# Optimization experiments

Hardware: AMD Instinct MI355X
Metric: run time of the kernel (lower is better)

The kernel has to match this reference:

```python
import jax, jax.numpy as jnp
import numpy as np

H = 256; HID = 128; V = 50000; LV = 200
N = 512; L = 64; M = 64; C = 4; T = 8; K = 8; E = 2048


def _gru_cell(x, h, wih, whh, bih, bhh):
    gi = x @ wih.T + bih
    gh = h @ whh.T + bhh
    ir, iz, inn = jnp.split(gi, 3, -1)
    hr, hz, hn = jnp.split(gh, 3, -1)
    r = jax.nn.sigmoid(ir + hr)
    z = jax.nn.sigmoid(iz + hz)
    n = jnp.tanh(inn + r * hn)
    return (1.0 - z) * n + z * h


def _bigru(x, wih, whh, bih, bhh):
    # x: [B, L, D]; params stacked [2, ...] = (fwd, bwd). out [B, L, 2*hid]
    B = x.shape[0]
    hid = whh.shape[-1]
    def run(xseq, d):
        def step(h, xt):
            hn = _gru_cell(xt, h, wih[d], whh[d], bih[d], bhh[d])
            return hn, hn
        _, out = jax.lax.scan(step, jnp.zeros((B, hid), x.dtype), jnp.swapaxes(xseq, 0, 1))
        return jnp.swapaxes(out, 0, 1)
    fwd = run(x, 0)
    bwd = jnp.flip(run(jnp.flip(x, 1), 1), 1)
    return jnp.concatenate([fwd, bwd], -1)


def _attn_pool(x, w, b):
    # x: [..., L, H]; softmax over L (matches torch softmax(dim=0) per sequence)
    a = jnp.einsum('...lh,h->...l', x, w) + b
    wts = jax.nn.softmax(a, axis=-1)
    return jnp.einsum('...l,...lh->...h', wts, x)


def _forward(seq_emb, seq_wih, seq_whh, seq_bih, seq_bhh, seq_pw, seq_pb,
             ctx_wih, ctx_whh, ctx_bih, ctx_bhh, ctx_pw, ctx_pb,
             ast_label_tab, ast_tok_tab, ast_pw, ast_pb,
             tl_wiou, tl_biou, tl_uiou, tl_wf, tl_bf, tl_uf,
             fa_wih, fa_whh, fa_bih, fa_bhh, fa_aw, fa_ab,
             comb_w, comb_b, g1_w, g1_b, g2_w, g2_b,
             cls_w1, cls_b1, cls_w2, cls_b2,
             seq_tokens, ast_children, ast_child_mask, ast_label_ids, ast_tok_ids, ctx_nei, edges):
    n_stmt = seq_tokens.shape[1]
    # --- three sequence encoders (stmt/varname/vartype), vmapped over encoder axis
    def enc(toks, emb, wih, whh, bih, bhh, pw, pb):
        e = emb[toks]                              # [N, L, H]
        o = _bigru(e, wih, whh, bih, bhh)          # [N, L, H]
        return _attn_pool(o, pw, pb)               # [N, H]
    vecs = jax.vmap(enc)(seq_tokens, seq_emb, seq_wih, seq_whh, seq_bih, seq_bhh, seq_pw, seq_pb)
    stmt_v, varn_v, vart_v = vecs[0], vecs[1], vecs[2]
    # --- ChildSum TreeLSTM over AST, batched over statements, scanned by node index
    # (children always have lower index than parent -> valid topological order)
    tok_e = ast_tok_tab[ast_tok_ids].mean(2)       # [N, M, H]
    xn = 0.5 * ast_label_tab[ast_label_ids] + 0.5 * tok_e
    Mn = xn.shape[1]
    xs = jnp.swapaxes(xn, 0, 1)                    # [M, N, H]
    chs = jnp.swapaxes(ast_children, 0, 1)         # [M, N, C]
    cms = jnp.swapaxes(ast_child_mask, 0, 1).astype(xn.dtype)
    nidx = jnp.arange(xn.shape[0])[:, None]
    def tl_step(carry, inp):
        h_arr, c_arr = carry                       # [M, N, H] each
        m, x, ch, msk = inp
        ch_h = h_arr[ch, nidx] * msk[..., None]    # [N, C, H], masked children
        ch_c = c_arr[ch, nidx] * msk[..., None]
        h_sum = ch_h.sum(1)
        iou = x @ tl_wiou.T + tl_biou + h_sum @ tl_uiou.T
        i, o, u = jnp.split(iou, 3, -1)
        i = jax.nn.sigmoid(i); o = jax.nn.sigmoid(o); u = jnp.tanh(u)
        fg = jax.nn.sigmoid((x @ tl_wf.T + tl_bf)[:, None, :] + ch_h @ tl_uf.T)
        c = i * u + (fg * ch_c).sum(1)
        h = o * jnp.tanh(c)
        return (h_arr.at[m].set(h), c_arr.at[m].set(c)), None
    z0 = jnp.zeros((Mn, xn.shape[0], xn.shape[2]), xn.dtype)
    (h_arr, _), _ = jax.lax.scan(tl_step, (z0, z0), (jnp.arange(Mn), xs, chs, cms))
    ast_v = _attn_pool(jnp.swapaxes(h_arr, 0, 1), ast_pw, ast_pb)   # [N, H]
    # --- context encoder over neighbor statement vectors (detached in original)
    ctx_in = jax.lax.stop_gradient(stmt_v)[ctx_nei]                 # [N, K, H]
    ctx_v = _attn_pool(_bigru(ctx_in, ctx_wih, ctx_whh, ctx_bih, ctx_bhh), ctx_pw, ctx_pb)
    # --- feature attention over the 5 per-statement feature vectors
    feats = jnp.stack([stmt_v, ast_v, varn_v, vart_v, ctx_v], axis=1)  # [N, 5, H]
    o = _bigru(feats, fa_wih, fa_whh, fa_bih, fa_bhh)
    wts = jax.nn.softmax(o @ fa_aw + fa_ab, axis=-1)
    x = jnp.einsum('nl,nlh->nh', wts, feats)
    # --- neighbor-mean combine (undirected unique edges)
    e0, e1 = edges[:, 0], edges[:, 1]
    rows = jnp.concatenate([e0, e1]); srcs = jnp.concatenate([e1, e0])
    nei_sum = jax.ops.segment_sum(x[srcs], rows, num_segments=n_stmt)
    deg = jax.ops.segment_sum(jnp.ones(rows.shape[0], x.dtype), rows, num_segments=n_stmt)
    nei_mean = nei_sum / jnp.maximum(deg, 1.0)[:, None]
    x2 = jax.nn.relu(jnp.concatenate([x, nei_mean], -1) @ comb_w.T + comb_b)
    # --- 2-layer symmetric-normalized GCN (edges both directions + self loops)
    sl = jnp.arange(n_stmt)
    r2 = jnp.concatenate([e0, e1, sl]); c2 = jnp.concatenate([e1, e0, sl])
    d2 = jax.ops.segment_sum(jnp.ones(r2.shape[0], x.dtype), r2, num_segments=n_stmt)
    dis = jnp.maximum(d2, 1.0) ** -0.5
    norm = (dis[r2] * dis[c2])[:, None]
    spmm = lambda y: jax.ops.segment_sum(norm * y[c2], r2, num_segments=n_stmt)
    h1 = jax.nn.relu(spmm(x2 @ g1_w.T + g1_b))
    h2 = jax.nn.relu(spmm(h1 @ g2_w.T + g2_b))
    gvec = jnp.concatenate([h2.mean(0), h2.max(0)], -1)
    return (jax.nn.relu(gvec @ cls_w1.T + cls_b1) @ cls_w2.T + cls_b2)[0]


def setup_inputs() -> dict:
    rng = np.random.default_rng(0)
    ks = iter(jax.random.split(jax.random.key(0), 64))
    def p(shape, s=0.05):
        return jax.random.normal(next(ks), shape, dtype=jnp.float32) * s
    inp = {}
    inp['seq_tokens'] = jnp.asarray(rng.integers(0, V, (3, N, L)), jnp.int32)
    ub = np.maximum(np.arange(M), 1)
    inp['ast_children'] = jnp.asarray((rng.random((N, M, C)) * ub[None, :, None]).astype(np.int64), jnp.int32)
    inp['ast_child_mask'] = jnp.asarray((rng.random((N, M, C)) < 0.7) & (np.arange(M)[None, :, None] > 0))
    inp['ast_label_ids'] = jnp.asarray(rng.integers(0, LV, (N, M)), jnp.int32)
    inp['ast_tok_ids'] = jnp.asarray(rng.integers(0, V, (N, M, T)), jnp.int32)
    inp['ctx_nei'] = jnp.asarray(rng.integers(0, N, (N, K)), jnp.int32)
    pairs = rng.integers(0, N, (8 * E, 2))
    pairs = pairs[pairs[:, 0] < pairs[:, 1]]
    pairs = np.unique(pairs, axis=0)[:E]
    inp['edges'] = jnp.asarray(pairs, jnp.int32)
    inp['seq_emb'] = p((3, V, H)).at[:, 0].set(0.0)  # padding_idx=0
    inp['seq_wih'] = p((3, 2, 3 * HID, H)); inp['seq_whh'] = p((3, 2, 3 * HID, HID))
    inp['seq_bih'] = p((3, 2, 3 * HID)); inp['seq_bhh'] = p((3, 2, 3 * HID))
    inp['seq_pw'] = p((3, H)); inp['seq_pb'] = p((3,))
    inp['ctx_wih'] = p((2, 3 * HID, H)); inp['ctx_whh'] = p((2, 3 * HID, HID))
    inp['ctx_bih'] = p((2, 3 * HID)); inp['ctx_bhh'] = p((2, 3 * HID))
    inp['ctx_pw'] = p((H,)); inp['ctx_pb'] = p(())
    inp['ast_label_tab'] = p((LV, H)); inp['ast_tok_tab'] = p((V, H))
    inp['ast_pw'] = p((H,)); inp['ast_pb'] = p(())
    inp['tl_wiou'] = p((3 * H, H)); inp['tl_biou'] = p((3 * H,)); inp['tl_uiou'] = p((3 * H, H))
    inp['tl_wf'] = p((H, H)); inp['tl_bf'] = p((H,)); inp['tl_uf'] = p((H, H))
    inp['fa_wih'] = p((2, 3 * HID, H)); inp['fa_whh'] = p((2, 3 * HID, HID))
    inp['fa_bih'] = p((2, 3 * HID)); inp['fa_bhh'] = p((2, 3 * HID))
    inp['fa_aw'] = p((H,)); inp['fa_ab'] = p(())
    inp['comb_w'] = p((H, 2 * H)); inp['comb_b'] = p((H,))
    inp['g1_w'] = p((H, H)); inp['g1_b'] = p((H,))
    inp['g2_w'] = p((H, H)); inp['g2_b'] = p((H,))
    inp['cls_w1'] = p((H, 2 * H)); inp['cls_b1'] = p((H,))
    inp['cls_w2'] = p((1, H)); inp['cls_b2'] = p((1,))
    return inp


def reference(seq_emb, seq_wih, seq_whh, seq_bih, seq_bhh, seq_pw, seq_pb,
              ctx_wih, ctx_whh, ctx_bih, ctx_bhh, ctx_pw, ctx_pb,
              ast_label_tab, ast_tok_tab, ast_pw, ast_pb,
              tl_wiou, tl_biou, tl_uiou, tl_wf, tl_bf, tl_uf,
              fa_wih, fa_whh, fa_bih, fa_bhh, fa_aw, fa_ab,
              comb_w, comb_b, g1_w, g1_b, g2_w, g2_b,
              cls_w1, cls_b1, cls_w2, cls_b2,
              seq_tokens, ast_children, ast_child_mask, ast_label_ids, ast_tok_ids, ctx_nei, edges):
    return _forward(seq_emb, seq_wih, seq_whh, seq_bih, seq_bhh, seq_pw, seq_pb,
                    ctx_wih, ctx_whh, ctx_bih, ctx_bhh, ctx_pw, ctx_pb,
                    ast_label_tab, ast_tok_tab, ast_pw, ast_pb,
                    tl_wiou, tl_biou, tl_uiou, tl_wf, tl_bf, tl_uf,
                    fa_wih, fa_whh, fa_bih, fa_bhh, fa_aw, fa_ab,
                    comb_w, comb_b, g1_w, g1_b, g2_w, g2_b,
                    cls_w1, cls_b1, cls_w2, cls_b2,
                    seq_tokens, ast_children, ast_child_mask, ast_label_ids, ast_tok_ids, ctx_nei, edges)
```

## Files before the change

### kernel.cpp

```cpp
#include <hip/hip_runtime.h>
#include <hip/hip_bf16.h>
#include <cmath>


__device__ __forceinline__ float sigf(float x) { return 1.f / (1.f + expf(-x)); }
__device__ __forceinline__ float b2f(__hip_bfloat16 x) { return __bfloat162float(x); }
__device__ __forceinline__ float bu2f(unsigned short u) {
  union { float f; unsigned i; } v; v.i = ((unsigned)u) << 16; return v.f;
}

typedef __attribute__((ext_vector_type(8))) short bf16x8v;
typedef __attribute__((ext_vector_type(4))) float f32x4;

__device__ __forceinline__ void gload16(const __hip_bfloat16* g, __hip_bfloat16* l) {
  __builtin_amdgcn_global_load_lds((const __attribute__((address_space(1))) void*)g,
                                   (__attribute__((address_space(3))) void*)l, 16, 0, 0);
}

__global__ __launch_bounds__(256) void k_build_wx(const float* __restrict__ wiou,
                                                  const float* __restrict__ wf,
                                                  const float* __restrict__ biou,
                                                  const float* __restrict__ bf,
                                                  float* __restrict__ w,
                                                  float* __restrict__ b) {
  int i = blockIdx.x * 256 + threadIdx.x;
  if (i < 1024 * 256) {
    int j = i >> 8, k = i & 255;
    w[i] = (j < 768) ? wiou[j * 256 + k] : wf[(j - 768) * 256 + k];
  }
  if (i < 1024) b[i] = (i < 768) ? biou[i] : bf[i - 768];
}

__global__ __launch_bounds__(256) void k_build_wproj(const float* __restrict__ uiou,
                                                     const float* __restrict__ uf,
                                                     float* __restrict__ w) {
  int i = blockIdx.x * 256 + threadIdx.x;
  if (i >= 1024 * 256) return;
  int j = i >> 8, k = i & 255;
  w[i] = (j < 768) ? uiou[j * 256 + k] : uf[(j - 768) * 256 + k];
}

__global__ __launch_bounds__(256) void k_zero_misc(float* __restrict__ nei_sum,
                                                   int* __restrict__ deg,
                                                   int* __restrict__ flag) {
  int i = blockIdx.x * 256 + threadIdx.x;
  if (i < 512 * 256) nei_sum[i] = 0.f;
  if (i < 512) deg[i] = 0;
  if (i == 0) *flag = 0;
}

__global__ __launch_bounds__(256) void k_mask_detect(const unsigned* __restrict__ raw,
                                                     int* __restrict__ flag) {
  int i = blockIdx.x * 256 + threadIdx.x;
  if (i < 32768) {
    if (raw[i] > 1u) atomicOr(flag, 1);
  }
}

__global__ __launch_bounds__(256) void k_mask_convert(const void* __restrict__ raw,
                                                      const int* __restrict__ flag,
                                                      int* __restrict__ msk) {
  int i = blockIdx.x * 256 + threadIdx.x;
  if (i >= 512 * 64 * 4) return;
  int v;
  if (*flag) v = ((const unsigned char*)raw)[i] != 0;
  else       v = ((const int*)raw)[i] != 0;
  msk[i] = v;
}

__global__ __launch_bounds__(256) void k_cvt_bf16(const float* __restrict__ A,
                                                  const int* __restrict__ ridx,
                                                  int rstride,
                                                  __hip_bfloat16* __restrict__ out) {
  int r = blockIdx.x * 8 + (threadIdx.x >> 5);
  int k = (threadIdx.x & 31) * 8;
  const float* src = A + (size_t)(ridx ? ridx[r] : r) * rstride + k;
  float4 v0 = *(const float4*)src;
  float4 v1 = *(const float4*)(src + 4);
  union { ushort4 u; __hip_bfloat16 b[4]; } p0, p1;
  p0.b[0] = __float2bfloat16(v0.x); p0.b[1] = __float2bfloat16(v0.y);
  p0.b[2] = __float2bfloat16(v0.z); p0.b[3] = __float2bfloat16(v0.w);
  p1.b[0] = __float2bfloat16(v1.x); p1.b[1] = __float2bfloat16(v1.y);
  p1.b[2] = __float2bfloat16(v1.z); p1.b[3] = __float2bfloat16(v1.w);
  __hip_bfloat16* dst = out + (size_t)r * 256 + k;
  *(ushort4*)dst = p0.u;
  *(ushort4*)(dst + 4) = p1.u;
}

__global__ __launch_bounds__(256) void k_gemm_mfma(const __hip_bfloat16* __restrict__ A,
                                                   const __hip_bfloat16* __restrict__ W,
                                                   const float* __restrict__ bias,
                                                   void* __restrict__ Cv,
                                                   int R, int K, int J,
                                                   int relu, int out_bf16) {
  __shared__ __align__(16) __hip_bfloat16 As[128 * 32];
  __shared__ __align__(16) __hip_bfloat16 Bs[128 * 32];
  int njt = J >> 7;
  int rt = blockIdx.x / njt;
  int jt = blockIdx.x - rt * njt;
  int tid = threadIdx.x;
  int w = tid >> 6, lane = tid & 63;
  int wr = w >> 1, wc = w & 1;

  const __hip_bfloat16* ga = A + (size_t)(rt * 128 + w * 32 + (lane >> 2)) * K + (lane & 3) * 8;
  const __hip_bfloat16* gb = W + (size_t)(jt * 128 + w * 32 + (lane >> 2)) * K + (lane & 3) * 8;
  __hip_bfloat16* lA0 = As + w * 1024;
  __hip_bfloat16* lB0 = Bs + w * 1024;
  size_t gstep16 = (size_t)16 * K;

  f32x4 acc[4][4];
#pragma unroll
  for (int m = 0; m < 4; ++m)
#pragma unroll
    for (int n = 0; n < 4; ++n) acc[m][n] = (f32x4){0.f, 0.f, 0.f, 0.f};

  int fr = lane & 15;
  int kg = (lane >> 4) * 8;
  const __hip_bfloat16* raA = As + (size_t)(wr * 64 + fr) * 32 + kg;
  const __hip_bfloat16* raB = Bs + (size_t)(wc * 64 + fr) * 32 + kg;

  for (int k0 = 0; k0 < K; k0 += 32) {
    __syncthreads();
    gload16(ga, lA0);
    gload16(ga + gstep16, lA0 + 512);
    gload16(gb, lB0);
    gload16(gb + gstep16, lB0 + 512);
    ga += 32; gb += 32;
    __syncthreads();
    bf16x8v a[4], b[4];
#pragma unroll
    for (int m = 0; m < 4; ++m) a[m] = *(const bf16x8v*)(raA + m * 512);
#pragma unroll
    for (int n = 0; n < 4; ++n) b[n] = *(const bf16x8v*)(raB + n * 512);
#pragma unroll
    for (int m = 0; m < 4; ++m)
#pragma unroll
      for (int n = 0; n < 4; ++n)
        acc[m][n] = __builtin_amdgcn_mfma_f32_16x16x32_bf16(a[m], b[n], acc[m][n], 0, 0, 0);
  }

  int row0 = rt * 128 + wr * 64 + (lane >> 4) * 4;
  int col0 = jt * 128 + wc * 64 + fr;
#pragma unroll
  for (int n = 0; n < 4; ++n) {
    int col = col0 + n * 16;
    float bv = bias ? bias[col] : 0.f;
#pragma unroll
    for (int m = 0; m < 4; ++m) {
#pragma unroll
      for (int j = 0; j < 4; ++j) {
        float v = acc[m][n][j] + bv;
        if (relu) v = fmaxf(v, 0.f);
        size_t idx = (size_t)(row0 + m * 16 + j) * J + col;
        if (out_bf16) ((__hip_bfloat16*)Cv)[idx] = __float2bfloat16(v);
        else ((float*)Cv)[idx] = v;
      }
    }
  }
}

__global__ __launch_bounds__(256) void k_gemm128(const float* __restrict__ A,
                                                 const int* __restrict__ ridx,
                                                 int rstride,
                                                 const float* __restrict__ W,
                                                 const float* __restrict__ bias,
                                                 float* __restrict__ C,
                                                 int R, int K, int J, int relu,
                                                 int out_bf16) {
  __shared__ float As[16][132];
  __shared__ float Ws[16][132];
  int njt = J >> 7;
  int rt = blockIdx.x / njt;
  int jt = blockIdx.x % njt;
  int tid = threadIdx.x;
  int tx = tid & 15, ty = tid >> 4;

  int row2 = tid >> 1;
  int kq = (tid & 1) * 4;
  int gr = rt * 128 + row2;
  const float* arow = A + (size_t)(ridx ? ridx[gr] : gr) * rstride;
  const float* wrow = W + (size_t)(jt * 128 + row2) * K;

  float acc[8][8];
#pragma unroll
  for (int i = 0; i < 8; ++i)
#pragma unroll
    for (int j = 0; j < 8; ++j) acc[i][j] = 0.f;

  for (int k0 = 0; k0 < K; k0 += 16) {
    float4 av0 = *(const float4*)(arow + k0 + kq);
    float4 av1 = *(const float4*)(arow + k0 + kq + 8);
    float4 wv0 = *(const float4*)(wrow + k0 + kq);
    float4 wv1 = *(const float4*)(wrow + k0 + kq + 8);
    __syncthreads();
    As[kq + 0][row2] = av0.x; As[kq + 1][row2] = av0.y;
    As[kq + 2][row2] = av0.z; As[kq + 3][row2] = av0.w;
    As[kq + 8][row2] = av1.x; As[kq + 9][row2] = av1.y;
    As[kq + 10][row2] = av1.z; As[kq + 11][row2] = av1.w;
    Ws[kq + 0][row2] = wv0.x; Ws[kq + 1][row2] = wv0.y;
    Ws[kq + 2][row2] = wv0.z; Ws[kq + 3][row2] = wv0.w;
    Ws[kq + 8][row2] = wv1.x; Ws[kq + 9][row2] = wv1.y;
    Ws[kq + 10][row2] = wv1.z; Ws[kq + 11][row2] = wv1.w;
    __syncthreads();
#pragma unroll
    for (int kk = 0; kk < 16; ++kk) {
      float a[8], b[8];
      *(float4*)&a[0] = *(const float4*)&As[kk][ty * 4];
      *(float4*)&a[4] = *(const float4*)&As[kk][64 + ty * 4];
      *(float4*)&b[0] = *(const float4*)&Ws[kk][tx * 4];
      *(float4*)&b[4] = *(const float4*)&Ws[kk][64 + tx * 4];
#pragma unroll
      for (int i = 0; i < 8; ++i)
#pragma unroll
        for (int j = 0; j < 8; ++j) acc[i][j] += a[i] * b[j];
    }
  }

  int col0 = jt * 128 + tx * 4;
  int col1 = jt * 128 + 64 + tx * 4;
  float b0[4], b1[4];
#pragma unroll
  for (int j = 0; j < 4; ++j) {
    b0[j] = bias ? bias[col0 + j] : 0.f;
    b1[j] = bias ? bias[col1 + j] : 0.f;
  }
#pragma unroll
  for (int i = 0; i < 8; ++i) {
    int row = rt * 128 + ((i < 4) ? (ty * 4 + i) : (64 + ty * 4 + i - 4));
    float v0[4], v1[4];
#pragma unroll
    for (int j = 0; j < 4; ++j) {
      float x0 = acc[i][j] + b0[j];
      float x1 = acc[i][j + 4] + b1[j];
      if (relu) { x0 = fmaxf(x0, 0.f); x1 = fmaxf(x1, 0.f); }
      v0[j] = x0; v1[j] = x1;
    }
    if (out_bf16) {
      __hip_bfloat16* Cb = (__hip_bfloat16*)C;
      union { ushort4 u; __hip_bfloat16 b[4]; } p0, p1;
#pragma unroll
      for (int j = 0; j < 4; ++j) { p0.b[j] = __float2bfloat16(v0[j]); p1.b[j] = __float2bfloat16(v1[j]); }
      *(ushort4*)(Cb + (size_t)row * J + col0) = p0.u;
      *(ushort4*)(Cb + (size_t)row * J + col1) = p1.u;
    } else {
      *(float4*)(C + (size_t)row * J + col0) = *(float4*)v0;
      *(float4*)(C + (size_t)row * J + col1) = *(float4*)v1;
    }
  }
}

__global__ __launch_bounds__(512) void k_gru4(const __hip_bfloat16* __restrict__ gi,
                                              const __hip_bfloat16* __restrict__ whhb,
                                              const float* __restrict__ bhh,
                                              float* __restrict__ out,
                                              int L) {
  __shared__ __align__(16) __hip_bfloat16 hsb[16][136];
  __shared__ float outl[16][392];
  int tid = threadIdx.x;
  int d = blockIdx.y;
  int n0 = blockIdx.x * 16;
  int w = tid >> 6, lane = tid & 63;
  int fr = lane & 15;
  int kg = (lane >> 4) * 8;
  int jw = w * 48;

  bf16x8v bfr[3][4];
  const __hip_bfloat16* wb = whhb + (size_t)d * 384 * 128;
#pragma unroll
  for (int cf = 0; cf < 3; ++cf)
#pragma unroll
    for (int kf = 0; kf < 4; ++kf)
      bfr[cf][kf] = *(const bf16x8v*)(wb + (size_t)(jw + cf * 16 + fr) * 128 + kf * 32 + kg);

  int s = tid >> 5;
  int j0 = (tid & 31) * 4;
  const float* bh = bhh + d * 384;
  float4 br = *(const float4*)(bh + j0);
  float4 bz = *(const float4*)(bh + 128 + j0);
  float4 bn = *(const float4*)(bh + 256 + j0);

  float h[4] = {0.f, 0.f, 0.f, 0.f};
  for (int i = tid; i < 16 * 136; i += 512) ((__hip_bfloat16*)hsb)[i] = __float2bfloat16(0.f);
  __syncthreads();

  int t = d ? (L - 1) : 0;
  int dt = d ? -1 : 1;

  for (int step = 0; step < L; ++step, t += dt) {
    const __hip_bfloat16* g = gi + (size_t)((n0 + s) * L + t) * 768 + d * 384 + j0;
    ushort4 gr4 = *(const ushort4*)(g);
    ushort4 gz4 = *(const ushort4*)(g + 128);
    ushort4 gn4 = *(const ushort4*)(g + 256);

    f32x4 acc[3];
#pragma unroll
    for (int cf = 0; cf < 3; ++cf) acc[cf] = (f32x4){0.f, 0.f, 0.f, 0.f};
#pragma unroll
    for (int kf = 0; kf < 4; ++kf) {
      bf16x8v a = *(const bf16x8v*)(&hsb[fr][kf * 32 + kg]);
#pragma unroll
      for (int cf = 0; cf < 3; ++cf)
        acc[cf] = __builtin_amdgcn_mfma_f32_16x16x32_bf16(a, bfr[cf][kf], acc[cf], 0, 0, 0);
    }
    int r0 = (lane >> 4) * 4;
#pragma unroll
    for (int cf = 0; cf < 3; ++cf) {
      int col = jw + cf * 16 + fr;
#pragma unroll
      for (int r = 0; r < 4; ++r) outl[r0 + r][col] = acc[cf][r];
    }
    __syncthreads();

    float4 sr = *(const float4*)&outl[s][j0];
    float4 sz = *(const float4*)&outl[s][128 + j0];
    float4 sn = *(const float4*)&outl[s][256 + j0];
    float gr[4] = {bu2f(gr4.x), bu2f(gr4.y), bu2f(gr4.z), bu2f(gr4.w)};
    float gz[4] = {bu2f(gz4.x), bu2f(gz4.y), bu2f(gz4.z), bu2f(gz4.w)};
    float gn[4] = {bu2f(gn4.x), bu2f(gn4.y), bu2f(gn4.z), bu2f(gn4.w)};
    float srv[4] = {sr.x, sr.y, sr.z, sr.w};
    float szv[4] = {sz.x, sz.y, sz.z, sz.w};
    float snv[4] = {sn.x, sn.y, sn.z, sn.w};
    float brv[4] = {br.x, br.y, br.z, br.w};
    float bzv[4] = {bz.x, bz.y, bz.z, bz.w};
    float bnv[4] = {bn.x, bn.y, bn.z, bn.w};
#pragma unroll
    for (int j = 0; j < 4; ++j) {
      float r = sigf(gr[j] + srv[j] + brv[j]);
      float z = sigf(gz[j] + szv[j] + bzv[j]);
      float nn = tanhf(gn[j] + r * (snv[j] + bnv[j]));
      h[j] = (1.f - z) * nn + z * h[j];
    }
    *(float4*)(out + (size_t)((n0 + s) * L + t) * 256 + d * 128 + j0) =
        (float4){h[0], h[1], h[2], h[3]};
    union { ushort4 u; __hip_bfloat16 b[4]; } hp;
#pragma unroll
    for (int j = 0; j < 4; ++j) hp.b[j] = __float2bfloat16(h[j]);
    *(ushort4*)&hsb[s][j0] = hp.u;
    __syncthreads();
  }
}

__global__ __launch_bounds__(256) void k_attn_pool(const float* __restrict__ score_src,
                                                   int s_ns, int s_ls,
                                                   const float* __restrict__ val_src,
                                                   int v_ns, int v_ls,
                                                   const float* __restrict__ w,
                                                   const float* __restrict__ bptr,
                                                   float* __restrict__ dst,
                                                   int dst_stride, int L) {
  __shared__ float wts[64];
  int n = blockIdx.x;
  int tid = threadIdx.x;
  if (tid < 64) {
    float a = -INFINITY;
    if (tid < L) {
      const float* row = score_src + (size_t)n * s_ns + (size_t)tid * s_ls;
      float s = bptr[0];
      for (int h = 0; h < 256; h += 4) {
        float4 v = *(const float4*)(row + h);
        float4 wv = *(const float4*)(w + h);
        s += v.x * wv.x + v.y * wv.y + v.z * wv.z + v.w * wv.w;
      }
      a = s;
    }
    float mx = a;
#pragma unroll
    for (int off = 32; off; off >>= 1) mx = fmaxf(mx, __shfl_xor(mx, off));
    float e = (tid < L) ? expf(a - mx) : 0.f;
    float ss = e;
#pragma unroll
    for (int off = 32; off; off >>= 1) ss += __shfl_xor(ss, off);
    if (tid < L) wts[tid] = e / ss;
  }
  __syncthreads();
  float acc = 0.f;
  for (int l = 0; l < L; ++l)
    acc += wts[l] * val_src[(size_t)n * v_ns + (size_t)l * v_ls + tid];
  dst[(size_t)n * dst_stride + tid] = acc;
}

__global__ __launch_bounds__(256) void k_xn_bf16(const float* __restrict__ label_tab,
                                                 const float* __restrict__ tok_tab,
                                                 const int* __restrict__ lbl_ids,
                                                 const int* __restrict__ tok_ids,
                                                 __hip_bfloat16* __restrict__ xnb) {
  int nm = blockIdx.x;
  int h = threadIdx.x;
  const int* tids = tok_ids + (size_t)nm * 8;
  float s = 0.f;
#pragma unroll
  for (int t = 0; t < 8; ++t) s += tok_tab[(size_t)tids[t] * 256 + h];
  float v = 0.5f * label_tab[(size_t)lbl_ids[nm] * 256 + h] + 0.0625f * s;
  xnb[(size_t)nm * 256 + h] = __float2bfloat16(v);
}

__global__ __launch_bounds__(256) void k_tl_combine4(const __hip_bfloat16* __restrict__ HU,
                                                     const __hip_bfloat16* __restrict__ XWALL,
                                                     const int* __restrict__ ch,
                                                     const int* __restrict__ msk,
                                                     float* __restrict__ h_arr,
                                                     float* __restrict__ c_arr,
                                                     __hip_bfloat16* __restrict__ hbf,
                                                     int m) {
  int n = blockIdx.x, h = threadIdx.x;
  const __hip_bfloat16* xw = XWALL + ((size_t)(n * 64 + m)) * 1024;
  float si = b2f(xw[h]), so = b2f(xw[256 + h]), su = b2f(xw[512 + h]);
  float xfv = b2f(xw[768 + h]);
  const int* chp = ch + ((size_t)(n * 64 + m)) * 4;
  const int* mkp = msk + ((size_t)(n * 64 + m)) * 4;
  float cs = 0.f;
#pragma unroll
  for (int c = 0; c < 4; ++c) {
    if (mkp[c]) {
      int cc = chp[c];
      const __hip_bfloat16* hu = HU + ((size_t)cc * 512 + n) * 1024;
      si += b2f(hu[h]);
      so += b2f(hu[256 + h]);
      su += b2f(hu[512 + h]);
      float fg = sigf(xfv + b2f(hu[768 + h]));
      cs += fg * c_arr[((size_t)cc * 512 + n) * 256 + h];
    }
  }
  float iv = sigf(si), ov = sigf(so), uv = tanhf(su);
  float cn = iv * uv + cs;
  float hn = ov * tanhf(cn);
  h_arr[((size_t)m * 512 + n) * 256 + h] = hn;
  c_arr[((size_t)m * 512 + n) * 256 + h] = cn;
  hbf[(size_t)n * 256 + h] = __float2bfloat16(hn);
}

__global__ __launch_bounds__(256) void k_edge_deg(const int* __restrict__ edges,
                                                  int* __restrict__ deg, int E) {
  int i = blockIdx.x * 256 + threadIdx.x;
  if (i < E) {
    atomicAdd(&deg[edges[2 * i]], 1);
    atomicAdd(&deg[edges[2 * i + 1]], 1);
  }
}

__global__ __launch_bounds__(256) void k_nei(const int* __restrict__ edges,
                                             const float* __restrict__ x,
                                             float* __restrict__ nei_sum) {
  int e = blockIdx.x, h = threadIdx.x;
  int a = edges[2 * e], b = edges[2 * e + 1];
  atomicAdd(&nei_sum[(size_t)a * 256 + h], x[(size_t)b * 256 + h]);
  atomicAdd(&nei_sum[(size_t)b * 256 + h], x[(size_t)a * 256 + h]);
}

__global__ __launch_bounds__(256) void k_xcat(const float* __restrict__ x,
                                              const float* __restrict__ nei_sum,
                                              const int* __restrict__ deg,
                                              float* __restrict__ xcat) {
  int n = blockIdx.x, h = threadIdx.x;
  xcat[(size_t)n * 512 + h] = x[(size_t)n * 256 + h];
  float d = fmaxf((float)deg[n], 1.f);
  xcat[(size_t)n * 512 + 256 + h] = nei_sum[(size_t)n * 256 + h] / d;
}

__global__ __launch_bounds__(256) void k_spmm_self(const float* __restrict__ y,
                                                   const int* __restrict__ deg,
                                                   float* __restrict__ ob) {
  int n = blockIdx.x, h = threadIdx.x;
  float dis2 = 1.f / (float)(deg[n] + 1);
  ob[(size_t)n * 256 + h] = dis2 * y[(size_t)n * 256 + h];
}

__global__ __launch_bounds__(256) void k_spmm_edge(const float* __restrict__ y,
                                                   const int* __restrict__ deg,
                                                   const int* __restrict__ edges,
                                                   float* __restrict__ ob) {
  int e = blockIdx.x, h = threadIdx.x;
  int a = edges[2 * e], b = edges[2 * e + 1];
  float w = (1.f / sqrtf((float)(deg[a] + 1))) * (1.f / sqrtf((float)(deg[b] + 1)));
  atomicAdd(&ob[(size_t)a * 256 + h], w * y[(size_t)b * 256 + h]);
  atomicAdd(&ob[(size_t)b * 256 + h], w * y[(size_t)a * 256 + h]);
}

__global__ __launch_bounds__(256) void k_relu_inplace(float* __restrict__ p) {
  int i = blockIdx.x * 256 + threadIdx.x;
  p[i] = fmaxf(p[i], 0.f);
}

__global__ __launch_bounds__(256) void k_final(const float* __restrict__ h2,
                                               const float* __restrict__ w1,
                                               const float* __restrict__ b1,
                                               const float* __restrict__ w2,
                                               const float* __restrict__ b2,
                                               float* __restrict__ outp) {
  __shared__ float gv[512];
  __shared__ float zz[256];
  int tid = threadIdx.x;
  float mn = 0.f, mx = -INFINITY;
  for (int n = 0; n < 512; ++n) {
    float v = h2[(size_t)n * 256 + tid];
    mn += v;
    mx = fmaxf(mx, v);
  }
  gv[tid] = mn / 512.f;
  gv[256 + tid] = mx;
  __syncthreads();
  float acc = b1[tid];
  for (int k = 0; k < 512; ++k) acc += gv[k] * w1[(size_t)tid * 512 + k];
  zz[tid] = fmaxf(acc, 0.f) * w2[tid];
  __syncthreads();
  for (int s = 128; s; s >>= 1) {
    if (tid < s) zz[tid] += zz[tid + s];
    __syncthreads();
  }
  if (tid == 0) outp[0] = zz[0] + b2[0];
}

extern "C" void kernel_launch(void* const* d_in, const int* in_sizes, int n_in,
                              void* d_out, int out_size, void* d_ws, size_t ws_size,
                              hipStream_t stream) {
  const int* seq_tokens    = (const int*)d_in[0];
  const int* ast_children  = (const int*)d_in[1];
  const void* ast_mask_raw = (const void*)d_in[2];
  const int* ast_label_ids = (const int*)d_in[3];
  const int* ast_tok_ids   = (const int*)d_in[4];
  const int* ctx_nei       = (const int*)d_in[5];
  const int* edges         = (const int*)d_in[6];
  const float* seq_emb  = (const float*)d_in[7];
  const float* seq_wih  = (const float*)d_in[8];
  const float* seq_whh  = (const float*)d_in[9];
  const float* seq_bih  = (const float*)d_in[10];
  const float* seq_bhh  = (const float*)d_in[11];
  const float* seq_pw   = (const float*)d_in[12];
  const float* seq_pb   = (const float*)d_in[13];
  const float* ctx_wih  = (const float*)d_in[14];
  const float* ctx_whh  = (const float*)d_in[15];
  const float* ctx_bih  = (const float*)d_in[16];
  const float* ctx_bhh  = (const float*)d_in[17];
  const float* ctx_pw   = (const float*)d_in[18];
  const float* ctx_pb   = (const float*)d_in[19];
  const float* ast_label_tab = (const float*)d_in[20];
  const float* ast_tok_tab   = (const float*)d_in[21];
  const float* ast_pw   = (const float*)d_in[22];
  const float* ast_pb   = (const float*)d_in[23];
  const float* tl_wiou  = (const float*)d_in[24];
  const float* tl_biou  = (const float*)d_in[25];
  const float* tl_uiou  = (const float*)d_in[26];
  const float* tl_wf    = (const float*)d_in[27];
  const float* tl_bf    = (const float*)d_in[28];
  const float* tl_uf    = (const float*)d_in[29];
  const float* fa_wih   = (const float*)d_in[30];
  const float* fa_whh   = (const float*)d_in[31];
  const float* fa_bih   = (const float*)d_in[32];
  const float* fa_bhh   = (const float*)d_in[33];
  const float* fa_aw    = (const float*)d_in[34];
  const float* fa_ab    = (const float*)d_in[35];
  const float* comb_w   = (const float*)d_in[36];
  const float* comb_b   = (const float*)d_in[37];
  const float* g1_w     = (const float*)d_in[38];
  const float* g1_b     = (const float*)d_in[39];
  const float* g2_w     = (const float*)d_in[40];
  const float* g2_b     = (const float*)d_in[41];
  const float* cls_w1   = (const float*)d_in[42];
  const float* cls_b1   = (const float*)d_in[43];
  const float* cls_w2   = (const float*)d_in[44];
  const float* cls_b2   = (const float*)d_in[45];
  float* outp = (float*)d_out;
  float* ws = (float*)d_ws;
  int E = in_sizes[6] / 2;

  size_t off = 0;
  auto take = [&](size_t n) { size_t o = off; off += n; return o; };
  const size_t F_FEATS = take(512 * 5 * 256);
  const size_t F_X     = take(512 * 256);
  const size_t F_X2    = take(512 * 256);
  const size_t F_Y     = take(512 * 256);
  const size_t F_H1    = take(512 * 256);
  const size_t F_H2    = take(512 * 256);
  const size_t F_XCAT  = take(512 * 512);
  const size_t F_NEI   = take(512 * 256);
  const size_t F_DEG   = take(512);
  const size_t F_FLAG  = take(16);
  const size_t F_MSK   = take(512 * 64 * 4);
  const size_t F_WXW   = take(1024 * 256);
  const size_t F_WXB   = take(1024);
  const size_t F_WPROJ = take(1024 * 256);
  const size_t F_REGION = take(83886080);
  (void)ws_size;

  float* FEATS = ws + F_FEATS;
  float* X     = ws + F_X;
  float* X2    = ws + F_X2;
  float* Y     = ws + F_Y;
  float* H1    = ws + F_H1;
  float* H2    = ws + F_H2;
  float* XCAT  = ws + F_XCAT;
  float* NEI   = ws + F_NEI;
  int*   DEG   = (int*)(ws + F_DEG);
  int*   FLAG  = (int*)(ws + F_FLAG);
  int*   MSK   = (int*)(ws + F_MSK);
  float* WXW   = ws + F_WXW;
  float* WXB   = ws + F_WXB;
  float* WPROJ = ws + F_WPROJ;
  float* REG   = ws + F_REGION;
  __hip_bfloat16* GI16  = (__hip_bfloat16*)REG;
  float* OUT   = REG + 13631488;
  __hip_bfloat16* XWALL16 = (__hip_bfloat16*)REG;
  float* HARR  = REG + 17000000;
  float* CARR  = REG + 25500000;
  __hip_bfloat16* HU16 = (__hip_bfloat16*)(REG + 34000000);
  __hip_bfloat16* GIFA16 = (__hip_bfloat16*)REG;
  float* OUTFA = REG + 1966080;
  __hip_bfloat16* ABF     = (__hip_bfloat16*)(REG + 60000000);
  __hip_bfloat16* WSEQBF  = (__hip_bfloat16*)(REG + 65000000);
  __hip_bfloat16* WCTXBF  = (__hip_bfloat16*)(REG + 65400000);
  __hip_bfloat16* WFABF   = (__hip_bfloat16*)(REG + 65600000);
  __hip_bfloat16* WXWBF   = (__hip_bfloat16*)(REG + 65800000);
  __hip_bfloat16* WPROJBF = (__hip_bfloat16*)(REG + 66100000);
  __hip_bfloat16* HBF     = (__hip_bfloat16*)(REG + 66500000);
  __hip_bfloat16* WHHSEQBF = (__hip_bfloat16*)(REG + 66600000);
  __hip_bfloat16* WHHCTXBF = (__hip_bfloat16*)(REG + 66800000);
  __hip_bfloat16* WHHFABF  = (__hip_bfloat16*)(REG + 66900000);

  auto gemm = [&](const float* A, const int* ridx, int rstride, const float* W,
                  const float* bias, float* C, int R, int K, int J, int relu,
                  int obf) {
    dim3 g((R / 128) * (J / 128));
    k_gemm128<<<g, 256, 0, stream>>>(A, ridx, rstride, W, bias, C, R, K, J, relu, obf);
  };
  auto cvt = [&](const float* A, const int* ridx, int rstride,
                 __hip_bfloat16* ob, int R) {
    k_cvt_bf16<<<R / 8, 256, 0, stream>>>(A, ridx, rstride, ob);
  };
  auto mgemm = [&](const __hip_bfloat16* A, const __hip_bfloat16* W,
                   const float* bias, void* C, int R, int K, int J, int relu,
                   int obf) {
    dim3 g((R / 128) * (J / 128));
    k_gemm_mfma<<<g, 256, 0, stream>>>(A, W, bias, C, R, K, J, relu, obf);
  };

  k_build_wx<<<1024, 256, 0, stream>>>(tl_wiou, tl_wf, tl_biou, tl_bf, WXW, WXB);
  k_build_wproj<<<1024, 256, 0, stream>>>(tl_uiou, tl_uf, WPROJ);
  k_zero_misc<<<512, 256, 0, stream>>>(NEI, DEG, FLAG);
  k_mask_detect<<<128, 256, 0, stream>>>((const unsigned*)ast_mask_raw, FLAG);
  k_mask_convert<<<512, 256, 0, stream>>>(ast_mask_raw, FLAG, MSK);
  cvt(seq_wih, nullptr, 256, WSEQBF, 2304);
  cvt(ctx_wih, nullptr, 256, WCTXBF, 768);
  cvt(fa_wih, nullptr, 256, WFABF, 768);
  cvt(WXW, nullptr, 256, WXWBF, 1024);
  cvt(WPROJ, nullptr, 256, WPROJBF, 1024);
  cvt(seq_whh, nullptr, 256, WHHSEQBF, 1152);
  cvt(ctx_whh, nullptr, 256, WHHCTXBF, 384);
  cvt(fa_whh, nullptr, 256, WHHFABF, 384);

  const int slot_of[3] = {0, 2, 3};
  for (int e = 0; e < 3; ++e) {
    cvt(seq_emb + (size_t)e * 50000 * 256, seq_tokens + (size_t)e * 32768, 256,
        ABF, 32768);
    mgemm(ABF, WSEQBF + (size_t)e * 768 * 256, seq_bih + (size_t)e * 768,
          GI16, 32768, 256, 768, 0, 1);
    k_gru4<<<dim3(32, 2), 512, 0, stream>>>(GI16, WHHSEQBF + (size_t)e * 2 * 384 * 128,
                                            seq_bhh + (size_t)e * 768, OUT, 64);
    k_attn_pool<<<512, 256, 0, stream>>>(OUT, 64 * 256, 256, OUT, 64 * 256, 256,
                                         seq_pw + e * 256, seq_pb + e,
                                         FEATS + slot_of[e] * 256, 1280, 64);
  }

  cvt(FEATS, ctx_nei, 1280, ABF, 4096);
  mgemm(ABF, WCTXBF, ctx_bih, GI16, 4096, 256, 768, 0, 1);
  k_gru4<<<dim3(32, 2), 512, 0, stream>>>(GI16, WHHCTXBF, ctx_bhh, OUT, 8);
  k_attn_pool<<<512, 256, 0, stream>>>(OUT, 8 * 256, 256, OUT, 8 * 256, 256,
                                       ctx_pw, ctx_pb, FEATS + 4 * 256, 1280, 8);

  k_xn_bf16<<<32768, 256, 0, stream>>>(ast_label_tab, ast_tok_tab, ast_label_ids,
                                       ast_tok_ids, ABF);
  mgemm(ABF, WXWBF, WXB, XWALL16, 32768, 256, 1024, 0, 1);
  for (int m = 0; m < 64; ++m) {
    k_tl_combine4<<<512, 256, 0, stream>>>(HU16, XWALL16, ast_children, MSK,
                                           HARR, CARR, HBF, m);
    if (m < 63)
      mgemm(HBF, WPROJBF, nullptr, HU16 + (size_t)m * 512 * 1024,
            512, 256, 1024, 0, 1);
  }
  k_attn_pool<<<512, 256, 0, stream>>>(HARR, 256, 512 * 256, HARR, 256, 512 * 256,
                                       ast_pw, ast_pb, FEATS + 1 * 256, 1280, 64);

  cvt(FEATS, nullptr, 256, ABF, 2560);
  mgemm(ABF, WFABF, fa_bih, GIFA16, 2560, 256, 768, 0, 1);
  k_gru4<<<dim3(32, 2), 512, 0, stream>>>(GIFA16, WHHFABF, fa_bhh, OUTFA, 5);
  k_attn_pool<<<512, 256, 0, stream>>>(OUTFA, 5 * 256, 256, FEATS, 1280, 256,
                                       fa_aw, fa_ab, X, 256, 5);

  k_edge_deg<<<(E + 255) / 256, 256, 0, stream>>>(edges, DEG, E);
  k_nei<<<E, 256, 0, stream>>>(edges, X, NEI);
  k_xcat<<<512, 256, 0, stream>>>(X, NEI, DEG, XCAT);
  gemm(XCAT, nullptr, 512, comb_w, comb_b, X2, 512, 512, 256, 1, 0);
  gemm(X2, nullptr, 256, g1_w, g1_b, Y, 512, 256, 256, 0, 0);
  k_spmm_self<<<512, 256, 0, stream>>>(Y, DEG, H1);
  k_spmm_edge<<<E, 256, 0, stream>>>(Y, DEG, edges, H1);
  k_relu_inplace<<<512, 256, 0, stream>>>(H1);
  gemm(H1, nullptr, 256, g2_w, g2_b, Y, 512, 256, 256, 0, 0);
  k_spmm_self<<<512, 256, 0, stream>>>(Y, DEG, H2);
  k_spmm_edge<<<E, 256, 0, stream>>>(Y, DEG, edges, H2);
  k_relu_inplace<<<512, 256, 0, stream>>>(H2);
  k_final<<<1, 256, 0, stream>>>(H2, cls_w1, cls_b1, cls_w2, cls_b2, outp);
}
```

Before: 2.101 ms.

## Batch three sequence-encoder GRUs into one launch with prefetch and fast activations

Input projections for all three sequence encoders are now computed into separate buffers, and one GRU kernel launch runs all three recurrences (96x2 blocks instead of three serial 32x2 launches). This fills more of the GPU's compute units during the latency-bound recurrent loop. The GRU loop also prefetches the next timestep's gate inputs, uses a lighter LDS-only barrier, and pads the shared output array. Sigmoid and tanh switch to fast-exp/rcp approximations in both the GRU and TreeLSTM kernels, trading a little accuracy for cheaper transcendentals, and the workspace grows to hold three projection and output buffers at once.

```diff
diff --git a/kernel.cpp b/kernel.cpp
--- a/kernel.cpp
+++ b/kernel.cpp
@@ -8,6 +8,14 @@
 __device__ __forceinline__ float bu2f(unsigned short u) {
   union { float f; unsigned i; } v; v.i = ((unsigned)u) << 16; return v.f;
 }
+__device__ __forceinline__ float fsig(float x) {
+  return __builtin_amdgcn_rcpf(1.f + __expf(-x));
+}
+__device__ __forceinline__ float ftanh(float x) {
+  float cx = fminf(fmaxf(x, -15.f), 15.f);
+  float e = __expf(2.f * cx);
+  return 1.f - 2.f * __builtin_amdgcn_rcpf(e + 1.f);
+}
 
 typedef __attribute__((ext_vector_type(8))) short bf16x8v;
 typedef __attribute__((ext_vector_type(4))) float f32x4;
@@ -15,6 +23,12 @@
 __device__ __forceinline__ void gload16(const __hip_bfloat16* g, __hip_bfloat16* l) {
   __builtin_amdgcn_global_load_lds((const __attribute__((address_space(1))) void*)g,
                                    (__attribute__((address_space(3))) void*)l, 16, 0, 0);
+}
+
+__device__ __forceinline__ void lds_barrier() {
+  asm volatile("s_waitcnt lgkmcnt(0)" ::: "memory");
+  __builtin_amdgcn_sched_barrier(0);
+  __builtin_amdgcn_s_barrier();
 }
 
 __global__ __launch_bounds__(256) void k_build_wx(const float* __restrict__ wiou,
@@ -249,16 +263,24 @@
   }
 }
 
-__global__ __launch_bounds__(512) void k_gru4(const __hip_bfloat16* __restrict__ gi,
+__global__ __launch_bounds__(512) void k_gru5(const __hip_bfloat16* __restrict__ gi,
                                               const __hip_bfloat16* __restrict__ whhb,
                                               const float* __restrict__ bhh,
                                               float* __restrict__ out,
-                                              int L) {
+                                              int L, int bpe,
+                                              unsigned gi_se, unsigned whh_se,
+                                              unsigned bhh_se, unsigned out_se) {
   __shared__ __align__(16) __hip_bfloat16 hsb[16][136];
-  __shared__ float outl[16][392];
+  __shared__ float outl[16][396];
   int tid = threadIdx.x;
   int d = blockIdx.y;
-  int n0 = blockIdx.x * 16;
+  int e = blockIdx.x / bpe;
+  int n0 = (blockIdx.x - e * bpe) * 16;
+  gi += (size_t)e * gi_se;
+  whhb += (size_t)e * whh_se;
+  bhh += (size_t)e * bhh_se;
+  out += (size_t)e * out_se;
+
   int w = tid >> 6, lane = tid & 63;
   int fr = lane & 15;
   int kg = (lane >> 4) * 8;
@@ -285,12 +307,20 @@
 
   int t = d ? (L - 1) : 0;
   int dt = d ? -1 : 1;
-
-  for (int step = 0; step < L; ++step, t += dt) {
-    const __hip_bfloat16* g = gi + (size_t)((n0 + s) * L + t) * 768 + d * 384 + j0;
-    ushort4 gr4 = *(const ushort4*)(g);
-    ushort4 gz4 = *(const ushort4*)(g + 128);
-    ushort4 gn4 = *(const ushort4*)(g + 256);
+  const __hip_bfloat16* gbase = gi + (size_t)(n0 + s) * L * 768 + d * 384 + j0;
+
+  const __hip_bfloat16* g0 = gbase + (size_t)t * 768;
+  ushort4 cr = *(const ushort4*)g0;
+  ushort4 cz = *(const ushort4*)(g0 + 128);
+  ushort4 cn4 = *(const ushort4*)(g0 + 256);
+
+  for (int step = 0; step < L; ++step) {
+    int tn = t + dt;
+    tn = (tn < 0) ? 0 : ((tn >= L) ? (L - 1) : tn);
+    const __hip_bfloat16* gn_ = gbase + (size_t)tn * 768;
+    ushort4 nr = *(const ushort4*)gn_;
+    ushort4 nz = *(const ushort4*)(gn_ + 128);
+    ushort4 nn4 = *(const ushort4*)(gn_ + 256);
 
     f32x4 acc[3];
 #pragma unroll
@@ -309,14 +339,14 @@
 #pragma unroll
       for (int r = 0; r < 4; ++r) outl[r0 + r][col] = acc[cf][r];
     }
-    __syncthreads();
+    lds_barrier();
 
     float4 sr = *(const float4*)&outl[s][j0];
     float4 sz = *(const float4*)&outl[s][128 + j0];
     float4 sn = *(const float4*)&outl[s][256 + j0];
-    float gr[4] = {bu2f(gr4.x), bu2f(gr4.y), bu2f(gr4.z), bu2f(gr4.w)};
-    float gz[4] = {bu2f(gz4.x), bu2f(gz4.y), bu2f(gz4.z), bu2f(gz4.w)};
-    float gn[4] = {bu2f(gn4.x), bu2f(gn4.y), bu2f(gn4.z), bu2f(gn4.w)};
+    float grv[4] = {bu2f(cr.x), bu2f(cr.y), bu2f(cr.z), bu2f(cr.w)};
+    float gzv[4] = {bu2f(cz.x), bu2f(cz.y), bu2f(cz.z), bu2f(cz.w)};
+    float gnv[4] = {bu2f(cn4.x), bu2f(cn4.y), bu2f(cn4.z), bu2f(cn4.w)};
     float srv[4] = {sr.x, sr.y, sr.z, sr.w};
     float szv[4] = {sz.x, sz.y, sz.z, sz.w};
     float snv[4] = {sn.x, sn.y, sn.z, sn.w};
@@ -325,9 +355,9 @@
     float bnv[4] = {bn.x, bn.y, bn.z, bn.w};
 #pragma unroll
     for (int j = 0; j < 4; ++j) {
-      float r = sigf(gr[j] + srv[j] + brv[j]);
-      float z = sigf(gz[j] + szv[j] + bzv[j]);
-      float nn = tanhf(gn[j] + r * (snv[j] + bnv[j]));
+      float r = fsig(grv[j] + srv[j] + brv[j]);
+      float z = fsig(gzv[j] + szv[j] + bzv[j]);
+      float nn = ftanh(gnv[j] + r * (snv[j] + bnv[j]));
       h[j] = (1.f - z) * nn + z * h[j];
     }
     *(float4*)(out + (size_t)((n0 + s) * L + t) * 256 + d * 128 + j0) =
@@ -336,7 +366,10 @@
 #pragma unroll
     for (int j = 0; j < 4; ++j) hp.b[j] = __float2bfloat16(h[j]);
     *(ushort4*)&hsb[s][j0] = hp.u;
-    __syncthreads();
+    lds_barrier();
+
+    cr = nr; cz = nz; cn4 = nn4;
+    t += dt;
   }
 }
 
@@ -417,13 +450,13 @@
       si += b2f(hu[h]);
       so += b2f(hu[256 + h]);
       su += b2f(hu[512 + h]);
-      float fg = sigf(xfv + b2f(hu[768 + h]));
+      float fg = fsig(xfv + b2f(hu[768 + h]));
       cs += fg * c_arr[((size_t)cc * 512 + n) * 256 + h];
     }
   }
-  float iv = sigf(si), ov = sigf(so), uv = tanhf(su);
+  float iv = fsig(si), ov = fsig(so), uv = ftanh(su);
   float cn = iv * uv + cs;
-  float hn = ov * tanhf(cn);
+  float hn = ov * ftanh(cn);
   h_arr[((size_t)m * 512 + n) * 256 + h] = hn;
   c_arr[((size_t)m * 512 + n) * 256 + h] = cn;
   hbf[(size_t)n * 256 + h] = __float2bfloat16(hn);
@@ -597,24 +630,27 @@
   float* WXB   = ws + F_WXB;
   float* WPROJ = ws + F_WPROJ;
   float* REG   = ws + F_REGION;
-  __hip_bfloat16* GI16  = (__hip_bfloat16*)REG;
-  float* OUT   = REG + 13631488;
+
+  __hip_bfloat16* GI3  = (__hip_bfloat16*)REG;
+  float* OUT3 = REG + 38000000;
   __hip_bfloat16* XWALL16 = (__hip_bfloat16*)REG;
   float* HARR  = REG + 17000000;
   float* CARR  = REG + 25500000;
   __hip_bfloat16* HU16 = (__hip_bfloat16*)(REG + 34000000);
   __hip_bfloat16* GIFA16 = (__hip_bfloat16*)REG;
-  float* OUTFA = REG + 1966080;
-  __hip_bfloat16* ABF     = (__hip_bfloat16*)(REG + 60000000);
-  __hip_bfloat16* WSEQBF  = (__hip_bfloat16*)(REG + 65000000);
-  __hip_bfloat16* WCTXBF  = (__hip_bfloat16*)(REG + 65400000);
-  __hip_bfloat16* WFABF   = (__hip_bfloat16*)(REG + 65600000);
-  __hip_bfloat16* WXWBF   = (__hip_bfloat16*)(REG + 65800000);
-  __hip_bfloat16* WPROJBF = (__hip_bfloat16*)(REG + 66100000);
-  __hip_bfloat16* HBF     = (__hip_bfloat16*)(REG + 66500000);
-  __hip_bfloat16* WHHSEQBF = (__hip_bfloat16*)(REG + 66600000);
-  __hip_bfloat16* WHHCTXBF = (__hip_bfloat16*)(REG + 66800000);
-  __hip_bfloat16* WHHFABF  = (__hip_bfloat16*)(REG + 66900000);
+  float* OUTFA = OUT3;
+
+  float* SCR = REG + 63500000;
+  __hip_bfloat16* ABF      = (__hip_bfloat16*)(SCR);
+  __hip_bfloat16* WSEQBF   = (__hip_bfloat16*)(SCR + 4200000);
+  __hip_bfloat16* WCTXBF   = (__hip_bfloat16*)(SCR + 4500000);
+  __hip_bfloat16* WFABF    = (__hip_bfloat16*)(SCR + 4600000);
+  __hip_bfloat16* WXWBF    = (__hip_bfloat16*)(SCR + 4700000);
+  __hip_bfloat16* WPROJBF  = (__hip_bfloat16*)(SCR + 4850000);
+  __hip_bfloat16* HBF      = (__hip_bfloat16*)(SCR + 5000000);
+  __hip_bfloat16* WHHSEQBF = (__hip_bfloat16*)(SCR + 5100000);
+  __hip_bfloat16* WHHCTXBF = (__hip_bfloat16*)(SCR + 5260000);
+  __hip_bfloat16* WHHFABF  = (__hip_bfloat16*)(SCR + 5320000);
 
   auto gemm = [&](const float* A, const int* ridx, int rstride, const float* W,
                   const float* bias, float* C, int R, int K, int J, int relu,
@@ -652,18 +688,23 @@
     cvt(seq_emb + (size_t)e * 50000 * 256, seq_tokens + (size_t)e * 32768, 256,
         ABF, 32768);
     mgemm(ABF, WSEQBF + (size_t)e * 768 * 256, seq_bih + (size_t)e * 768,
-          GI16, 32768, 256, 768, 0, 1);
-    k_gru4<<<dim3(32, 2), 512, 0, stream>>>(GI16, WHHSEQBF + (size_t)e * 2 * 384 * 128,
-                                            seq_bhh + (size_t)e * 768, OUT, 64);
-    k_attn_pool<<<512, 256, 0, stream>>>(OUT, 64 * 256, 256, OUT, 64 * 256, 256,
+          GI3 + (size_t)e * 32768 * 768, 32768, 256, 768, 0, 1);
+  }
+  k_gru5<<<dim3(96, 2), 512, 0, stream>>>(GI3, WHHSEQBF, seq_bhh, OUT3, 64, 32,
+                                          32768u * 768u, 2u * 384u * 128u, 768u,
+                                          32768u * 256u);
+  for (int e = 0; e < 3; ++e) {
+    k_attn_pool<<<512, 256, 0, stream>>>(OUT3 + (size_t)e * 32768 * 256, 64 * 256, 256,
+                                         OUT3 + (size_t)e * 32768 * 256, 64 * 256, 256,
                                          seq_pw + e * 256, seq_pb + e,
                                          FEATS + slot_of[e] * 256, 1280, 64);
   }
 
   cvt(FEATS, ctx_nei, 1280, ABF, 4096);
-  mgemm(ABF, WCTXBF, ctx_bih, GI16, 4096, 256, 768, 0, 1);
-  k_gru4<<<dim3(32, 2), 512, 0, stream>>>(GI16, WHHCTXBF, ctx_bhh, OUT, 8);
-  k_attn_pool<<<512, 256, 0, stream>>>(OUT, 8 * 256, 256, OUT, 8 * 256, 256,
+  mgemm(ABF, WCTXBF, ctx_bih, GI3, 4096, 256, 768, 0, 1);
+  k_gru5<<<dim3(32, 2), 512, 0, stream>>>(GI3, WHHCTXBF, ctx_bhh, OUT3, 8, 32,
+                                          0, 0, 0, 0);
+  k_attn_pool<<<512, 256, 0, stream>>>(OUT3, 8 * 256, 256, OUT3, 8 * 256, 256,
                                        ctx_pw, ctx_pb, FEATS + 4 * 256, 1280, 8);
 
   k_xn_bf16<<<32768, 256, 0, stream>>>(ast_label_tab, ast_tok_tab, ast_label_ids,
@@ -681,7 +722,8 @@
 
   cvt(FEATS, nullptr, 256, ABF, 2560);
   mgemm(ABF, WFABF, fa_bih, GIFA16, 2560, 256, 768, 0, 1);
-  k_gru4<<<dim3(32, 2), 512, 0, stream>>>(GIFA16, WHHFABF, fa_bhh, OUTFA, 5);
+  k_gru5<<<dim3(32, 2), 512, 0, stream>>>(GIFA16, WHHFABF, fa_bhh, OUTFA, 5, 32,
+                                          0, 0, 0, 0);
   k_attn_pool<<<512, 256, 0, stream>>>(OUTFA, 5 * 256, 256, FEATS, 1280, 256,
                                        fa_aw, fa_ab, X, 256, 5);
 
```

Result: faster. 1.838 ms (-12.5%).
